# Kernel tuning notes

Measured on AMD Instinct MI355X. Metric: run time of the kernel, lower is better.

Reference implementation:

```python
import jax, jax.numpy as jnp
import numpy as np

T, B, D = 8192, 8, 512
PRIOR_COUNT = 2
EPS = 1e-5


def setup_inputs() -> dict:
    key = jax.random.key(0)
    ks = jax.random.split(key, 5)
    x = jax.random.normal(ks[0], (T, B, D), dtype=jnp.float32)
    padding_mask = jnp.zeros((B, T), dtype=bool)  # True = padded position
    prior_mean = jax.random.normal(ks[1], (D,), dtype=jnp.float32) * 0.1
    prior_logv = jax.random.normal(ks[2], (D,), dtype=jnp.float32) * 0.1
    weight = jax.random.normal(ks[3], (D,), dtype=jnp.float32) * 0.1
    bias = jax.random.normal(ks[4], (D,), dtype=jnp.float32) * 0.1
    return {"x": x, "prior_mean": prior_mean, "prior_logv": prior_logv,
            "weight": weight, "bias": bias, "padding_mask": padding_mask}


def reference(x, prior_mean, prior_logv, weight, bias, padding_mask):
    # x: (T, B, D); padding_mask: (B, T) with True = pad.
    # Per-timestep Welford running mean/variance (carried across time, skipping
    # padded steps) followed by affine normalization: the TimestepNorm forward.
    gamma = weight + 1.0
    beta = bias
    b = x.shape[1]
    count0 = jnp.full((b,), PRIOR_COUNT, dtype=x.dtype)
    mean0 = jnp.broadcast_to(prior_mean, (b, D)).astype(x.dtype)
    var0 = jnp.broadcast_to(jnp.exp(prior_logv), (b, D)).astype(x.dtype)
    mask_tb = padding_mask.T  # (T, B)

    def step(carry, inp):
        count, mean, var = carry
        xt, mt = inp                                  # xt: (B, D), mt: (B,)
        valid = (~mt).astype(xt.dtype)                # 1 if real token, 0 if pad
        c_new = count + valid
        coef = valid / c_new                          # 0 on padded steps
        delta = xt - mean
        mean_new = mean + coef[:, None] * delta
        # Welford variance update: var += (delta*(x - mean_new) - var)/count
        var_new = var + coef[:, None] * (delta * (xt - mean_new) - var)
        y = (xt - mean_new) * jax.lax.rsqrt(var_new + EPS) * gamma + beta
        return (c_new, mean_new, var_new), y

    (_, _, _), ys = jax.lax.scan(step, (count0, mean0, var0), (x, mask_tb))
    return ys  # (T, B, D), same layout as module output
```

## Files before the change

kernel.cpp:

```cpp
#include <hip/hip_runtime.h>
#include <math.h>


#define T_DIM 8192
#define B_DIM 8
#define D_DIM 512
#define BD    (B_DIM * D_DIM)
#define BD4   (BD / 4)
#define D4    (D_DIM / 4)
#define C0    2.0f
#define EPS   1e-5f

typedef float nt_f4 __attribute__((ext_vector_type(4)));

__device__ __forceinline__ float4 f4add(float4 a, float4 b) {
  return make_float4(a.x + b.x, a.y + b.y, a.z + b.z, a.w + b.w);
}
__device__ __forceinline__ float4 f4sub(float4 a, float4 b) {
  return make_float4(a.x - b.x, a.y - b.y, a.z - b.z, a.w - b.w);
}

__device__ __forceinline__ void ntstore4(float4 v, float4* p) {
  nt_f4 t = {v.x, v.y, v.z, v.w};
  __builtin_nontemporal_store(t, (nt_f4*)p);
}

template <int NC>
__global__ __launch_bounds__(128) void ts_pass1(
    const float* __restrict__ x, const unsigned char* __restrict__ mask,
    float* __restrict__ s1p, float* __restrict__ s2p, float* __restrict__ cnt) {
  constexpr int CT = T_DIM / NC;
  constexpr int NW = CT / 8;
  const int chunk = blockIdx.x;
  const int b     = blockIdx.y;
  const int tid   = threadIdx.x;
  const int t0    = chunk * CT;
  const float4* xp = (const float4*)x;

  unsigned long long mw[NW];
  const unsigned long long* m8 =
      (const unsigned long long*)(mask + b * T_DIM + t0);
#pragma unroll
  for (int j = 0; j < NW; ++j) mw[j] = m8[j];

  float4 s1 = make_float4(0.f, 0.f, 0.f, 0.f);
  float4 s2 = make_float4(0.f, 0.f, 0.f, 0.f);
  float c = 0.f;
#pragma unroll 8
  for (int i = 0; i < CT; ++i) {
    float valid = ((mw[i >> 3] >> ((i & 7) * 8)) & 0xffULL) ? 0.f : 1.f;
    float4 v = xp[(t0 + i) * BD4 + b * D4 + tid];
    c += valid;
    s1.x += valid * v.x; s2.x += valid * v.x * v.x;
    s1.y += valid * v.y; s2.y += valid * v.y * v.y;
    s1.z += valid * v.z; s2.z += valid * v.z * v.z;
    s1.w += valid * v.w; s2.w += valid * v.w * v.w;
  }
  const int pidx = chunk * BD4 + b * D4 + tid;
  ((float4*)s1p)[pidx] = s1;
  ((float4*)s2p)[pidx] = s2;
  if (tid == 0) cnt[chunk * B_DIM + b] = c;
}

template <int NC>
__global__ __launch_bounds__(256) void ts_pass2(
    float* __restrict__ s1p, float* __restrict__ s2p, float* __restrict__ cnt) {
  constexpr int KPL = NC / 64;
  const int wid  = (blockIdx.x * 256 + threadIdx.x) >> 6;
  const int lane = threadIdx.x & 63;

  if (wid < 2 * BD4) {
    float4* base = (float4*)(wid < BD4 ? s1p : s2p);
    const int col = wid & (BD4 - 1);
    float4 vals[KPL];
#pragma unroll
    for (int j = 0; j < KPL; ++j)
      vals[j] = base[(lane * KPL + j) * BD4 + col];
#pragma unroll
    for (int j = 1; j < KPL; ++j) vals[j] = f4add(vals[j], vals[j - 1]);
    float4 tot = vals[KPL - 1];
    float4 inc = tot;
#pragma unroll
    for (int off = 1; off < 64; off <<= 1) {
      float4 o;
      o.x = __shfl_up(inc.x, off);
      o.y = __shfl_up(inc.y, off);
      o.z = __shfl_up(inc.z, off);
      o.w = __shfl_up(inc.w, off);
      if (lane >= off) inc = f4add(inc, o);
    }
    float4 excl = f4sub(inc, tot);
#pragma unroll
    for (int j = KPL - 1; j >= 1; --j)
      base[(lane * KPL + j) * BD4 + col] = f4add(excl, vals[j - 1]);
    base[(lane * KPL) * BD4 + col] = excl;
  } else if (wid < 2 * BD4 + B_DIM) {
    const int b = wid - 2 * BD4;
    float vals[KPL];
#pragma unroll
    for (int j = 0; j < KPL; ++j) vals[j] = cnt[(lane * KPL + j) * B_DIM + b];
#pragma unroll
    for (int j = 1; j < KPL; ++j) vals[j] += vals[j - 1];
    float tot = vals[KPL - 1];
    float inc = tot;
#pragma unroll
    for (int off = 1; off < 64; off <<= 1) {
      float o = __shfl_up(inc, off);
      if (lane >= off) inc += o;
    }
    float excl = inc - tot;
#pragma unroll
    for (int j = KPL - 1; j >= 1; --j)
      cnt[(lane * KPL + j) * B_DIM + b] = excl + vals[j - 1];
    cnt[lane * KPL * B_DIM + b] = excl;
  }
}

template <int NC>
__global__ __launch_bounds__(128) void ts_pass3(
    const float* __restrict__ x, const unsigned char* __restrict__ mask,
    const float* __restrict__ pm, const float* __restrict__ plv,
    const float* __restrict__ w, const float* __restrict__ bias,
    const float* __restrict__ e1, const float* __restrict__ e2,
    const float* __restrict__ ecnt, float* __restrict__ out) {
  constexpr int CT = T_DIM / NC;
  constexpr int NW = CT / 8;
  const int chunk = blockIdx.x;
  const int b     = blockIdx.y;
  const int tid   = threadIdx.x;
  const int t0    = chunk * CT;
  const int col   = b * D4 + tid;

  float4 S1 = ((const float4*)e1)[chunk * BD4 + col];
  float4 S2 = ((const float4*)e2)[chunk * BD4 + col];
  float c = C0 + ecnt[chunk * B_DIM + b];

  float4 pm4 = ((const float4*)pm)[tid];
  float4 lv4 = ((const float4*)plv)[tid];
  float4 g4  = ((const float4*)w)[tid];
  float4 be4 = ((const float4*)bias)[tid];
  g4.x += 1.f; g4.y += 1.f; g4.z += 1.f; g4.w += 1.f;
  float M0x = C0 * pm4.x, M0y = C0 * pm4.y, M0z = C0 * pm4.z, M0w = C0 * pm4.w;
  float V2x = C0 * (__expf(lv4.x) + pm4.x * pm4.x);
  float V2y = C0 * (__expf(lv4.y) + pm4.y * pm4.y);
  float V2z = C0 * (__expf(lv4.z) + pm4.z * pm4.z);
  float V2w = C0 * (__expf(lv4.w) + pm4.w * pm4.w);

  unsigned long long mw[NW];
  const unsigned long long* m8 =
      (const unsigned long long*)(mask + b * T_DIM + t0);
#pragma unroll
  for (int j = 0; j < NW; ++j) mw[j] = m8[j];

  const float4* xp = (const float4*)x;
  float4* op = (float4*)out;

#pragma unroll 4
  for (int i = 0; i < CT; ++i) {
    float valid = ((mw[i >> 3] >> ((i & 7) * 8)) & 0xffULL) ? 0.f : 1.f;
    const int xi = (t0 + i) * BD4 + col;
    float4 v = xp[xi];
    c += valid;
    float rc = __builtin_amdgcn_rcpf(c);
    float4 y;
    {
      S1.x += valid * v.x; S2.x += valid * v.x * v.x;
      float M = M0x + S1.x;
      float mean = M * rc;
      float var = (V2x + S2.x - M * M * rc) * rc;
      y.x = (v.x - mean) * __builtin_amdgcn_rsqf(var + EPS) * g4.x + be4.x;
    }
    {
      S1.y += valid * v.y; S2.y += valid * v.y * v.y;
      float M = M0y + S1.y;
      float mean = M * rc;
      float var = (V2y + S2.y - M * M * rc) * rc;
      y.y = (v.y - mean) * __builtin_amdgcn_rsqf(var + EPS) * g4.y + be4.y;
    }
    {
      S1.z += valid * v.z; S2.z += valid * v.z * v.z;
      float M = M0z + S1.z;
      float mean = M * rc;
      float var = (V2z + S2.z - M * M * rc) * rc;
      y.z = (v.z - mean) * __builtin_amdgcn_rsqf(var + EPS) * g4.z + be4.z;
    }
    {
      S1.w += valid * v.w; S2.w += valid * v.w * v.w;
      float M = M0w + S1.w;
      float mean = M * rc;
      float var = (V2w + S2.w - M * M * rc) * rc;
      y.w = (v.w - mean) * __builtin_amdgcn_rsqf(var + EPS) * g4.w + be4.w;
    }
    ntstore4(y, &op[xi]);
  }
}

template <int NC>
static void run_3pass(const float* x, const unsigned char* mask,
                      const float* pm, const float* plv, const float* w,
                      const float* bias, float* out, float* ws,
                      hipStream_t stream) {
  float* s1p = ws;
  float* s2p = s1p + (size_t)NC * BD;
  float* cnt = s2p + (size_t)NC * BD;
  dim3 grid(NC, B_DIM);
  ts_pass1<NC><<<grid, 128, 0, stream>>>(x, mask, s1p, s2p, cnt);
  const int scan_waves = 2 * BD4 + B_DIM;
  const int scan_blocks = (scan_waves + 3) / 4;
  ts_pass2<NC><<<scan_blocks, 256, 0, stream>>>(s1p, s2p, cnt);
  ts_pass3<NC><<<grid, 128, 0, stream>>>(x, mask, pm, plv, w, bias, s1p, s2p,
                                         cnt, out);
}

extern "C" void kernel_launch(void* const* d_in, const int* in_sizes, int n_in,
                              void* d_out, int out_size, void* d_ws,
                              size_t ws_size, hipStream_t stream) {
  const float* x    = (const float*)d_in[0];
  const float* pm   = (const float*)d_in[1];
  const float* plv  = (const float*)d_in[2];
  const float* w    = (const float*)d_in[3];
  const float* bias = (const float*)d_in[4];
  const unsigned char* mask = (const unsigned char*)d_in[5];
  float* out = (float*)d_out;
  float* ws  = (float*)d_ws;

  const size_t need512 = ((size_t)2 * 512 * BD + 512 * B_DIM) * sizeof(float);
  const size_t need256 = ((size_t)2 * 256 * BD + 256 * B_DIM) * sizeof(float);
  if (ws_size >= need512) {
    run_3pass<512>(x, mask, pm, plv, w, bias, out, ws, stream);
  } else if (ws_size >= need256) {
    run_3pass<256>(x, mask, pm, plv, w, bias, out, ws, stream);
  } else {
    run_3pass<128>(x, mask, pm, plv, w, bias, out, ws, stream);
  }
}
```

Before: 276.6 us.

## Scan chunk partials at super-chunk granularity, finish prefix in pass3

```diff
diff --git a/kernel.cpp b/kernel.cpp
--- a/kernel.cpp
+++ b/kernel.cpp
@@ -11,6 +11,12 @@
 #define C0    2.0f
 #define EPS   1e-5f
 
+#define NCF   512
+#define CTF   (T_DIM / NCF)
+#define NWF   (CTF / 8)
+#define G     16
+#define NSC   (NCF / G)
+
 typedef float nt_f4 __attribute__((ext_vector_type(4)));
 
 __device__ __forceinline__ float4 f4add(float4 a, float4 b) {
@@ -19,35 +25,31 @@
 __device__ __forceinline__ float4 f4sub(float4 a, float4 b) {
   return make_float4(a.x - b.x, a.y - b.y, a.z - b.z, a.w - b.w);
 }
-
 __device__ __forceinline__ void ntstore4(float4 v, float4* p) {
   nt_f4 t = {v.x, v.y, v.z, v.w};
   __builtin_nontemporal_store(t, (nt_f4*)p);
 }
 
-template <int NC>
 __global__ __launch_bounds__(128) void ts_pass1(
     const float* __restrict__ x, const unsigned char* __restrict__ mask,
     float* __restrict__ s1p, float* __restrict__ s2p, float* __restrict__ cnt) {
-  constexpr int CT = T_DIM / NC;
-  constexpr int NW = CT / 8;
   const int chunk = blockIdx.x;
   const int b     = blockIdx.y;
   const int tid   = threadIdx.x;
-  const int t0    = chunk * CT;
+  const int t0    = chunk * CTF;
   const float4* xp = (const float4*)x;
 
-  unsigned long long mw[NW];
+  unsigned long long mw[NWF];
   const unsigned long long* m8 =
       (const unsigned long long*)(mask + b * T_DIM + t0);
 #pragma unroll
-  for (int j = 0; j < NW; ++j) mw[j] = m8[j];
+  for (int j = 0; j < NWF; ++j) mw[j] = m8[j];
 
   float4 s1 = make_float4(0.f, 0.f, 0.f, 0.f);
   float4 s2 = make_float4(0.f, 0.f, 0.f, 0.f);
   float c = 0.f;
-#pragma unroll 8
-  for (int i = 0; i < CT; ++i) {
+#pragma unroll
+  for (int i = 0; i < CTF; ++i) {
     float valid = ((mw[i >> 3] >> ((i & 7) * 8)) & 0xffULL) ? 0.f : 1.f;
     float4 v = xp[(t0 + i) * BD4 + b * D4 + tid];
     c += valid;
@@ -62,23 +64,22 @@
   if (tid == 0) cnt[chunk * B_DIM + b] = c;
 }
 
-template <int NC>
-__global__ __launch_bounds__(256) void ts_pass2(
-    float* __restrict__ s1p, float* __restrict__ s2p, float* __restrict__ cnt) {
-  constexpr int KPL = NC / 64;
+__global__ __launch_bounds__(256) void ts_pass2sup(
+    const float* __restrict__ s1p, const float* __restrict__ s2p,
+    const float* __restrict__ cnt, float* __restrict__ sup1,
+    float* __restrict__ sup2, float* __restrict__ supc) {
+  constexpr int KPL = NCF / 64;
   const int wid  = (blockIdx.x * 256 + threadIdx.x) >> 6;
   const int lane = threadIdx.x & 63;
 
   if (wid < 2 * BD4) {
-    float4* base = (float4*)(wid < BD4 ? s1p : s2p);
+    const float4* base = (const float4*)(wid < BD4 ? s1p : s2p);
+    float4* supo = (float4*)(wid < BD4 ? sup1 : sup2);
     const int col = wid & (BD4 - 1);
-    float4 vals[KPL];
+    float4 tot = make_float4(0.f, 0.f, 0.f, 0.f);
 #pragma unroll
     for (int j = 0; j < KPL; ++j)
-      vals[j] = base[(lane * KPL + j) * BD4 + col];
-#pragma unroll
-    for (int j = 1; j < KPL; ++j) vals[j] = f4add(vals[j], vals[j - 1]);
-    float4 tot = vals[KPL - 1];
+      tot = f4add(tot, base[(lane * KPL + j) * BD4 + col]);
     float4 inc = tot;
 #pragma unroll
     for (int off = 1; off < 64; off <<= 1) {
@@ -89,51 +90,58 @@
       o.w = __shfl_up(inc.w, off);
       if (lane >= off) inc = f4add(inc, o);
     }
-    float4 excl = f4sub(inc, tot);
-#pragma unroll
-    for (int j = KPL - 1; j >= 1; --j)
-      base[(lane * KPL + j) * BD4 + col] = f4add(excl, vals[j - 1]);
-    base[(lane * KPL) * BD4 + col] = excl;
+    float4 prev;
+    prev.x = __shfl_up(inc.x, 1);
+    prev.y = __shfl_up(inc.y, 1);
+    prev.z = __shfl_up(inc.z, 1);
+    prev.w = __shfl_up(inc.w, 1);
+    if ((lane & 1) == 0) {
+      float4 e = (lane == 0) ? make_float4(0.f, 0.f, 0.f, 0.f) : prev;
+      supo[(lane >> 1) * BD4 + col] = e;
+    }
   } else if (wid < 2 * BD4 + B_DIM) {
     const int b = wid - 2 * BD4;
-    float vals[KPL];
-#pragma unroll
-    for (int j = 0; j < KPL; ++j) vals[j] = cnt[(lane * KPL + j) * B_DIM + b];
-#pragma unroll
-    for (int j = 1; j < KPL; ++j) vals[j] += vals[j - 1];
-    float tot = vals[KPL - 1];
+    float tot = 0.f;
+#pragma unroll
+    for (int j = 0; j < KPL; ++j) tot += cnt[(lane * KPL + j) * B_DIM + b];
     float inc = tot;
 #pragma unroll
     for (int off = 1; off < 64; off <<= 1) {
       float o = __shfl_up(inc, off);
       if (lane >= off) inc += o;
     }
-    float excl = inc - tot;
-#pragma unroll
-    for (int j = KPL - 1; j >= 1; --j)
-      cnt[(lane * KPL + j) * B_DIM + b] = excl + vals[j - 1];
-    cnt[lane * KPL * B_DIM + b] = excl;
-  }
-}
-
-template <int NC>
+    float prev = __shfl_up(inc, 1);
+    if ((lane & 1) == 0)
+      supc[(lane >> 1) * B_DIM + b] = (lane == 0) ? 0.f : prev;
+  }
+}
+
 __global__ __launch_bounds__(128) void ts_pass3(
     const float* __restrict__ x, const unsigned char* __restrict__ mask,
     const float* __restrict__ pm, const float* __restrict__ plv,
     const float* __restrict__ w, const float* __restrict__ bias,
-    const float* __restrict__ e1, const float* __restrict__ e2,
-    const float* __restrict__ ecnt, float* __restrict__ out) {
-  constexpr int CT = T_DIM / NC;
-  constexpr int NW = CT / 8;
+    const float* __restrict__ s1p, const float* __restrict__ s2p,
+    const float* __restrict__ cnt, const float* __restrict__ sup1,
+    const float* __restrict__ sup2, const float* __restrict__ supc,
+    float* __restrict__ out) {
   const int chunk = blockIdx.x;
   const int b     = blockIdx.y;
   const int tid   = threadIdx.x;
-  const int t0    = chunk * CT;
+  const int t0    = chunk * CTF;
   const int col   = b * D4 + tid;
-
-  float4 S1 = ((const float4*)e1)[chunk * BD4 + col];
-  float4 S2 = ((const float4*)e2)[chunk * BD4 + col];
-  float c = C0 + ecnt[chunk * B_DIM + b];
+  const int sc    = chunk >> 4;
+
+  float4 S1 = ((const float4*)sup1)[sc * BD4 + col];
+  float4 S2 = ((const float4*)sup2)[sc * BD4 + col];
+  float csum = supc[sc * B_DIM + b];
+  for (int j = sc * G; j < chunk; ++j) {
+    float4 a = ((const float4*)s1p)[j * BD4 + col];
+    float4 d = ((const float4*)s2p)[j * BD4 + col];
+    S1 = f4add(S1, a);
+    S2 = f4add(S2, d);
+    csum += cnt[j * B_DIM + b];
+  }
+  float c = C0 + csum;
 
   float4 pm4 = ((const float4*)pm)[tid];
   float4 lv4 = ((const float4*)plv)[tid];
@@ -146,17 +154,17 @@
   float V2z = C0 * (__expf(lv4.z) + pm4.z * pm4.z);
   float V2w = C0 * (__expf(lv4.w) + pm4.w * pm4.w);
 
-  unsigned long long mw[NW];
+  unsigned long long mw[NWF];
   const unsigned long long* m8 =
       (const unsigned long long*)(mask + b * T_DIM + t0);
 #pragma unroll
-  for (int j = 0; j < NW; ++j) mw[j] = m8[j];
+  for (int j = 0; j < NWF; ++j) mw[j] = m8[j];
 
   const float4* xp = (const float4*)x;
   float4* op = (float4*)out;
 
 #pragma unroll 4
-  for (int i = 0; i < CT; ++i) {
+  for (int i = 0; i < CTF; ++i) {
     float valid = ((mw[i >> 3] >> ((i & 7) * 8)) & 0xffULL) ? 0.f : 1.f;
     const int xi = (t0 + i) * BD4 + col;
     float4 v = xp[xi];
@@ -193,23 +201,6 @@
     }
     ntstore4(y, &op[xi]);
   }
-}
-
-template <int NC>
-static void run_3pass(const float* x, const unsigned char* mask,
-                      const float* pm, const float* plv, const float* w,
-                      const float* bias, float* out, float* ws,
-                      hipStream_t stream) {
-  float* s1p = ws;
-  float* s2p = s1p + (size_t)NC * BD;
-  float* cnt = s2p + (size_t)NC * BD;
-  dim3 grid(NC, B_DIM);
-  ts_pass1<NC><<<grid, 128, 0, stream>>>(x, mask, s1p, s2p, cnt);
-  const int scan_waves = 2 * BD4 + B_DIM;
-  const int scan_blocks = (scan_waves + 3) / 4;
-  ts_pass2<NC><<<scan_blocks, 256, 0, stream>>>(s1p, s2p, cnt);
-  ts_pass3<NC><<<grid, 128, 0, stream>>>(x, mask, pm, plv, w, bias, s1p, s2p,
-                                         cnt, out);
 }
 
 extern "C" void kernel_launch(void* const* d_in, const int* in_sizes, int n_in,
@@ -224,13 +215,19 @@
   float* out = (float*)d_out;
   float* ws  = (float*)d_ws;
 
-  const size_t need512 = ((size_t)2 * 512 * BD + 512 * B_DIM) * sizeof(float);
-  const size_t need256 = ((size_t)2 * 256 * BD + 256 * B_DIM) * sizeof(float);
-  if (ws_size >= need512) {
-    run_3pass<512>(x, mask, pm, plv, w, bias, out, ws, stream);
-  } else if (ws_size >= need256) {
-    run_3pass<256>(x, mask, pm, plv, w, bias, out, ws, stream);
-  } else {
-    run_3pass<128>(x, mask, pm, plv, w, bias, out, ws, stream);
-  }
-}
+  float* s1p  = ws;
+  float* s2p  = s1p + (size_t)NCF * BD;
+  float* cnt  = s2p + (size_t)NCF * BD;
+  float* sup1 = cnt + (size_t)NCF * B_DIM;
+  float* sup2 = sup1 + (size_t)NSC * BD;
+  float* supc = sup2 + (size_t)NSC * BD;
+
+  dim3 grid(NCF, B_DIM);
+  ts_pass1<<<grid, 128, 0, stream>>>(x, mask, s1p, s2p, cnt);
+  const int scan_waves = 2 * BD4 + B_DIM;
+  const int scan_blocks = (scan_waves + 3) / 4;
+  ts_pass2sup<<<scan_blocks, 256, 0, stream>>>(s1p, s2p, cnt, sup1, sup2,
+                                               supc);
+  ts_pass3<<<grid, 128, 0, stream>>>(x, mask, pm, plv, w, bias, s1p, s2p, cnt,
+                                     sup1, sup2, supc, out);
+}
```

After: 287.2 us. 1.04x slower.
